# Kernel optimization log

Hardware: AMD Instinct MI355X
Metric: run time of the kernel (lower is better)

## Reference

```python
import jax, jax.numpy as jnp
from jax import lax
import numpy as np

P = 9  # patch_size


def unfold9(img):
    # img: (C, H, W) -> (C, P*P, L) with L = (H//P)*(W//P), non-overlapping patches
    C, H, W = img.shape
    x = img.reshape(C, H // P, P, W // P, P)
    x = x.transpose(0, 2, 4, 1, 3).reshape(C, P * P, (H // P) * (W // P))
    return x


def fold9(blocks, H, W):
    # blocks: (C, P*P, L) -> (C, H, W), inverse of unfold9 (no overlaps)
    C = blocks.shape[0]
    x = blocks.reshape(C, P, P, H // P, W // P)
    return x.transpose(0, 3, 1, 4, 2).reshape(C, H, W)


def avgpool3d_k3s2p1(x):
    # AvgPool3d(kernel=3, stride=2, padding=1, count_include_pad=False) on (B,C,D,H,W)
    win = (1, 1, 3, 3, 3)
    strides = (1, 1, 2, 2, 2)
    pad = [(0, 0), (0, 0), (1, 1), (1, 1), (1, 1)]
    s = lax.reduce_window(x, 0.0, lax.add, win, strides, pad)
    cnt = lax.reduce_window(jnp.ones_like(x[:1, :1]), 0.0, lax.add, win, strides, pad)
    return s / cnt


def setup_inputs() -> dict:
    key = jax.random.key(0)
    k = jax.random.split(key, 7)
    in1, in2, out = 32, 64, 64
    x = jax.random.normal(k[0], (1, in1, 36, 72, 72), jnp.float32)
    y = jax.random.normal(k[1], (1, in2, 18, 36, 36), jnp.float32)
    z = jax.random.normal(k[2], (1, out, 36, 72, 72), jnp.float32)
    w_img = jax.random.normal(k[3], (out, in1), jnp.float32) * 0.05
    b_img = jax.random.normal(k[4], (out,), jnp.float32) * 0.01
    w_fea = jax.random.normal(k[5], (out, in2), jnp.float32) * 0.05
    b_fea = jax.random.normal(k[6], (out,), jnp.float32) * 0.01
    return {"x": x, "y": y, "z": z, "w_img": w_img, "b_img": b_img,
            "w_fea": w_fea, "b_fea": b_fea}


def reference(x, y, z, w_img, b_img, w_fea, b_fea):
    # 1x1x1 conv projections (pointwise channel mix)
    xq = jnp.einsum('bcdhw,oc->bodhw', x, w_img) + b_img[None, :, None, None, None]
    yk = jnp.einsum('bcdhw,oc->bodhw', y, w_fea) + b_fea[None, :, None, None, None]
    C = xq.shape[1]
    D1, HW1 = xq.shape[2], xq.shape[3] * xq.shape[4]
    D2, HW2 = yk.shape[2], yk.shape[3] * yk.shape[4]
    Ux = unfold9(xq.reshape(C, D1, HW1))          # (C, 81, L1)
    Uy = unfold9(yk.reshape(C, D2, HW2))          # (C, 81, L2)
    att = jnp.einsum('ckl,ckm->clm', Ux, Uy)      # (C, L1, L2) per-channel patch attn

    # --- Cross_head ---
    Dd, Hd, Wd = z.shape[2], z.shape[3], z.shape[4]
    dec = z.reshape(C, Dd, Hd * Wd)               # decoder_reshape
    xd = avgpool3d_k3s2p1(z)                      # (1, C, Dd', Hd', Wd')
    Dp, HWp = xd.shape[2], xd.shape[3] * xd.shape[4]
    Uxd = unfold9(xd.reshape(C, Dp, HWp))         # (C, 81, L2)
    # count_nonzero along L2 (non-differentiable, matches torch)
    nz = jnp.sum(att != 0, axis=-1).astype(att.dtype) + 1e-5  # (C, L1)
    corr_blocks = jnp.einsum('clm,ckm->ckl', att / nz[:, :, None], Uxd)  # (C, 81, L1)
    corr = fold9(corr_blocks, Dd, Hd * Wd)        # (C, Dd, Hd*Wd)
    act = jnp.where(corr > 0, corr, 0.2 * corr)   # LeakyReLU(0.2)
    out = act * dec + dec
    return out.reshape(z.shape)
```

## Files before the change

kernel.cpp:

```cpp
#include <hip/hip_runtime.h>
#include <hip/hip_bf16.h>

typedef __hip_bfloat16 bf16;
typedef float in_t;
typedef float out_t;
typedef __attribute__((ext_vector_type(8))) short short8;
typedef __attribute__((ext_vector_type(4))) float f32x4;

#define CH    64
#define CIN1  32
#define CIN2  64
#define S1    186624
#define W1    5184
#define S2    23328
#define W2    1296
#define LDSTR 1297
#define BSTR  104
#define OSTR  136
#define YSTR  68
#define HWSTR 76
#define INV_NZ (1.0f/(288.0f + 1e-5f))

#define NB_PL 2304
#define NB_PX 1458
#define NB_PY 365
#define NBT   (NB_PL + NB_PX + NB_PY)
#define NBR   (NBT - NB_PL)

static __device__ __forceinline__ unsigned short f2bu(float f) {
    bf16 h = __float2bfloat16(f);
    unsigned short u;
    __builtin_memcpy(&u, &h, 2);
    return u;
}
static __device__ __forceinline__ float bu2f(unsigned short u) {
    unsigned int v = ((unsigned int)u) << 16;
    float f;
    __builtin_memcpy(&f, &v, 4);
    return f;
}

__global__ __launch_bounds__(256) void k_stage1(
    const in_t* __restrict__ x, const in_t* __restrict__ wi, const in_t* __restrict__ bi,
    bf16* __restrict__ xq,
    const in_t* __restrict__ y, const in_t* __restrict__ wf, const in_t* __restrict__ bf,
    unsigned short* __restrict__ yk,
    const in_t* __restrict__ z, unsigned short* __restrict__ xd)
{
    __shared__ __align__(16) char smem[17408];
    int t = threadIdx.x;
    long long i = blockIdx.x;

    long long pb = (i*NB_PL)/NBT;
    bool is_pool = ((i+1)*NB_PL)/NBT > pb;
    long long r  = i - pb;
    long long yb = (r*NB_PY)/NBR;
    bool is_py   = !is_pool && (((r+1)*NB_PY)/NBR > yb);

    if (is_pool) {
        int bid = (int)pb;
        float* dsum = reinterpret_cast<float*>(smem);
        int c  = bid / 36;
        int rr = bid - c*36;
        int od = rr >> 1, half = rr & 1;
        int hbase = half ? 35 : 0;
        int nrows = half ? 37 : 36;
        int oh0   = half ? 18 : 0;
        int dlo = od ? 2*od - 1 : 0;
        int nd  = od ? 3 : 2;
        const float* zb = z + ((size_t)c*36 + dlo)*W1;
        for (int ii = t; ii < nrows*18; ii += 256) {
            int rw = ii / 18, q = ii - (ii/18)*18;
            int off = (hbase + rw)*18 + q;
            const float4* p0 = reinterpret_cast<const float4*>(zb);
            float4 a = p0[off], b = p0[1296 + off];
            float4 s;
            if (nd == 3) {
                float4 e = p0[2592 + off];
                s = (float4){ a.x+b.x+e.x, a.y+b.y+e.y, a.z+b.z+e.z, a.w+b.w+e.w };
            } else {
                s = (float4){ a.x+b.x, a.y+b.y, a.z+b.z, a.w+b.w };
            }
            *reinterpret_cast<float4*>(&dsum[rw*HWSTR + q*4]) = s;
        }
        __syncthreads();
        float icd = (nd == 3) ? (1.f/3.f) : 0.5f;
        unsigned short* xdp = xd + (size_t)c*S2 + (size_t)od*W2 + oh0*36;
        for (int idx = t; idx < 648; idx += 256) {
            int ohl = idx / 36, ow = idx - (idx/36)*36;
            int oh = oh0 + ohl;
            int h0 = oh ? 2*oh-1 : 0, h1 = 2*oh+1;
            int w0 = ow ? 2*ow-1 : 0, w1 = 2*ow+1;
            float s = 0.f;
            for (int h = h0; h <= h1; ++h) {
                int lr = h - hbase;
                for (int w = w0; w <= w1; ++w)
                    s += dsum[lr*HWSTR + w];
            }
            float ich = (h1 - h0) == 1 ? 0.5f : (1.f/3.f);
            float icw = (w1 - w0) == 1 ? 0.5f : (1.f/3.f);
            xdp[idx] = f2bu(s * icd * ich * icw);
        }
    } else if (!is_py) {
        int gs0 = (int)(r - yb)*128;
        int l = t & 63, wv = t >> 6;
        int lcol = l & 15, loct = l >> 4;

        ushort4 rr4[2][4];
        #pragma unroll
        for (int mt = 0; mt < 2; ++mt) {
            int scol = gs0 + (wv*2 + mt)*16 + lcol;
            union { short8 v; unsigned short u[8]; } af;
            #pragma unroll
            for (int j = 0; j < 8; ++j)
                af.u[j] = f2bu(x[(size_t)(loct*8 + j)*S1 + scol]);
            #pragma unroll
            for (int og = 0; og < 4; ++og) {
                int o = og*16 + lcol;
                union { short8 v; unsigned short u[8]; } wfr;
                float4 a  = *reinterpret_cast<const float4*>(&wi[o*CIN1 + loct*8]);
                float4 bq = *reinterpret_cast<const float4*>(&wi[o*CIN1 + loct*8 + 4]);
                wfr.u[0]=f2bu(a.x);  wfr.u[1]=f2bu(a.y);
                wfr.u[2]=f2bu(a.z);  wfr.u[3]=f2bu(a.w);
                wfr.u[4]=f2bu(bq.x); wfr.u[5]=f2bu(bq.y);
                wfr.u[6]=f2bu(bq.z); wfr.u[7]=f2bu(bq.w);
                float bo = bi[o];
                f32x4 d = { bo, bo, bo, bo };
                d = __builtin_amdgcn_mfma_f32_16x16x32_bf16(af.v, wfr.v, d, 0, 0, 0);
                rr4[mt][og] = (ushort4){ f2bu(d[0]), f2bu(d[1]), f2bu(d[2]), f2bu(d[3]) };
            }
        }
        unsigned short* ot = reinterpret_cast<unsigned short*>(smem);
        #pragma unroll
        for (int mt = 0; mt < 2; ++mt)
            #pragma unroll
            for (int og = 0; og < 4; ++og)
                *reinterpret_cast<ushort4*>(
                    &ot[(og*16 + lcol)*OSTR + wv*32 + mt*16 + loct*4]) = rr4[mt][og];
        __syncthreads();
        #pragma unroll
        for (int j = 0; j < 4; ++j) {
            int row = wv*16 + j*4 + (l >> 4);
            int c8  = l & 15;
            uint4 v = *reinterpret_cast<const uint4*>(&ot[row*OSTR + c8*8]);
            *reinterpret_cast<uint4*>(
                (unsigned short*)xq + (size_t)row*S1 + gs0 + c8*8) = v;
        }
    } else {
        int pyb   = (int)yb;
        int sblk0 = pyb*64;
        int wv = t >> 6, l = t & 63;
        int lcol = l & 15, loct = l >> 4;
        int tile = pyb*4 + wv;
        unsigned short* ot = reinterpret_cast<unsigned short*>(smem);
        if (tile < 1458) {
            int s0 = tile*16;
            union { short8 v; unsigned short u[8]; } af[2];
            #pragma unroll
            for (int kk = 0; kk < 2; ++kk)
                #pragma unroll
                for (int j = 0; j < 8; ++j)
                    af[kk].u[j] = f2bu(y[(size_t)(kk*32 + loct*8 + j)*S2 + s0 + lcol]);
            #pragma unroll
            for (int og = 0; og < 4; ++og) {
                int o = og*16 + lcol;
                union { short8 v; unsigned short u[8]; } wfr[2];
                #pragma unroll
                for (int kk = 0; kk < 2; ++kk) {
                    float4 a  = *reinterpret_cast<const float4*>(&wf[o*CIN2 + kk*32 + loct*8]);
                    float4 bq = *reinterpret_cast<const float4*>(&wf[o*CIN2 + kk*32 + loct*8 + 4]);
                    wfr[kk].u[0]=f2bu(a.x);  wfr[kk].u[1]=f2bu(a.y);
                    wfr[kk].u[2]=f2bu(a.z);  wfr[kk].u[3]=f2bu(a.w);
                    wfr[kk].u[4]=f2bu(bq.x); wfr[kk].u[5]=f2bu(bq.y);
                    wfr[kk].u[6]=f2bu(bq.z); wfr[kk].u[7]=f2bu(bq.w);
                }
                float bo = bf[o];
                f32x4 d = { bo, bo, bo, bo };
                d = __builtin_amdgcn_mfma_f32_16x16x32_bf16(af[0].v, wfr[0].v, d, 0, 0, 0);
                d = __builtin_amdgcn_mfma_f32_16x16x32_bf16(af[1].v, wfr[1].v, d, 0, 0, 0);
                ushort4 r4 = { f2bu(d[0]), f2bu(d[1]), f2bu(d[2]), f2bu(d[3]) };
                *reinterpret_cast<ushort4*>(&ot[(og*16 + lcol)*YSTR + wv*16 + loct*4]) = r4;
            }
        }
        __syncthreads();
        #pragma unroll
        for (int j = 0; j < 4; ++j) {
            int row = wv*16 + j*4 + (l >> 4);
            int c4  = l & 15;
            int s   = sblk0 + c4*4;
            if (s < S2) {
                ushort4 v = *reinterpret_cast<const ushort4*>(&ot[row*YSTR + c4*4]);
                *reinterpret_cast<ushort4*>(&yk[(size_t)row*S2 + s]) = v;
            }
        }
    }
}

__global__ __launch_bounds__(256) void k_M(
    const unsigned short* __restrict__ xd, const unsigned short* __restrict__ yk,
    unsigned short* __restrict__ Mg)
{
    __shared__ float xl[3*LDSTR];
    __shared__ float yl[3*LDSTR];
    int b = blockIdx.x;
    int c = b / 9, r = b - c*9;
    int g = r / 3, h = r - g*3;
    int t = threadIdx.x;
    int t1 = t / 27, t2 = t - (t/27)*27;
    int offx[3];
    #pragma unroll
    for (int a = 0; a < 3; ++a) {
        int kl = t1*3 + a;
        offx[a] = (kl/9)*LDSTR + (kl - (kl/9)*9);
    }
    int offy = (t2/9)*LDSTR + (t2 - (t2/9)*9);
    float acc[3] = {};
    for (int ph2 = 0; ph2 < 2; ++ph2) {
        __syncthreads();
        for (int idx = t; idx < 3*W2; idx += 256) {
            int rr = idx / W2, col = idx - rr*W2;
            xl[rr*LDSTR + col] = bu2f(xd[c*S2 + (ph2*9 + g*3 + rr)*W2 + col]);
            yl[rr*LDSTR + col] = bu2f(yk[c*S2 + (ph2*9 + h*3 + rr)*W2 + col]);
        }
        __syncthreads();
        if (t < 243) {
            for (int m = 0; m < 144; ++m) {
                int cb = m*9;
                float yv = yl[cb + offy];
                #pragma unroll
                for (int a = 0; a < 3; ++a)
                    acc[a] += xl[cb + offx[a]] * yv;
            }
        }
    }
    if (t < 243) {
        #pragma unroll
        for (int a = 0; a < 3; ++a) {
            int k1 = g*27 + t1*3 + a;
            Mg[c*9216 + k1*96 + (h*27 + t2)] = f2bu(acc[a]);
        }
    }
    if (r == 0) {
        for (int idx = t; idx < 2655; idx += 256) {
            int row, col;
            if (idx < 1440) { int q = idx/96; row = 81 + q; col = idx - q*96; }
            else { int j = idx - 1440; int q = j/15; row = q; col = 81 + (j - q*15); }
            Mg[c*9216 + row*96 + col] = 0;
        }
    }
}

__global__ __launch_bounds__(256, 4) void k_corr(
    const unsigned short* __restrict__ Mg, const bf16* __restrict__ xq,
    const in_t* __restrict__ z, out_t* __restrict__ out)
{
    __shared__ __align__(16) unsigned short Pl[192*BSTR];
    int bid = blockIdx.x;
    int c   = bid / 12;
    int rem = bid - c*12;
    int ph  = rem / 3;
    int ck  = rem - ph*3;
    int colbase = ck*1728;
    int t = threadIdx.x;

    for (int idx = t; idx < 192*15; idx += 256) {
        int r = idx/15;
        Pl[r*BSTR + 81 + (idx - r*15)] = 0;
    }
    const unsigned short* xqu =
        (const unsigned short*)(xq + (size_t)c*S1 + (size_t)(ph*9)*W1 + colbase);
    for (int idx = t; idx < 3888; idx += 256) {
        int i2 = idx / 432, v4 = idx - i2*432;
        ushort4 vv = *reinterpret_cast<const ushort4*>(xqu + (size_t)i2*W1 + v4*4);
        int col = v4*4;
        unsigned short uu[4] = {vv.x, vv.y, vv.z, vv.w};
        #pragma unroll
        for (int j = 0; j < 4; ++j) {
            int cc = col + j;
            int p = cc/9, j2 = cc - p*9;
            Pl[p*BSTR + i2*9 + j2] = uu[j];
        }
    }
    __syncthreads();

    int wv = t >> 6, l = t & 63;
    int lrow = l & 15, lhi = l >> 4;

    short8 bfr[3][3];
    #pragma unroll
    for (int ntl = 0; ntl < 3; ++ntl) {
        int n = (wv*3 + ntl)*16 + lrow;
        #pragma unroll
        for (int kk = 0; kk < 3; ++kk)
            bfr[ntl][kk] = *reinterpret_cast<const short8*>(&Pl[n*BSTR + kk*32 + lhi*8]);
    }

    f32x4 acc[6][3];
    #pragma unroll
    for (int mt = 0; mt < 6; ++mt)
        #pragma unroll
        for (int ntl = 0; ntl < 3; ++ntl)
            acc[mt][ntl] = (f32x4){0.f,0.f,0.f,0.f};

    const unsigned short* Mc = Mg + c*9216;
    #pragma unroll
    for (int mt = 0; mt < 6; ++mt) {
        short8 afr[3];
        #pragma unroll
        for (int kk = 0; kk < 3; ++kk)
            afr[kk] = *reinterpret_cast<const short8*>(Mc + (mt*16 + lrow)*96 + kk*32 + lhi*8);
        #pragma unroll
        for (int ntl = 0; ntl < 3; ++ntl) {
            f32x4 d = acc[mt][ntl];
            #pragma unroll
            for (int kk = 0; kk < 3; ++kk)
                d = __builtin_amdgcn_mfma_f32_16x16x32_bf16(afr[kk], bfr[ntl][kk], d, 0, 0, 0);
            acc[mt][ntl] = d;
        }
    }
    __syncthreads();

    float* stage = reinterpret_cast<float*>(Pl);
    #pragma unroll
    for (int pass = 0; pass < 2; ++pass) {
        if ((wv >> 1) == pass) {
            #pragma unroll
            for (int mt = 0; mt < 6; ++mt)
                #pragma unroll
                for (int ntl = 0; ntl < 3; ++ntl) {
                    int n = (wv*3 + ntl)*16 + lrow - pass*96;
                    #pragma unroll
                    for (int r = 0; r < 4; ++r) {
                        int m = mt*16 + lhi*4 + r;
                        if (m <= 80) {
                            int i = m/9, j = m - 9*i;
                            stage[i*864 + n*9 + j] = acc[mt][ntl][r];
                        }
                    }
                }
        }
        __syncthreads();
        for (int idx = t; idx < 1944; idx += 256) {
            int i = idx/216, c4 = idx - i*216;
            float4 sv = *reinterpret_cast<const float4*>(&stage[i*864 + c4*4]);
            int ga = c*S1 + (ph*9 + i)*W1 + colbase + pass*864 + c4*4;
            float4 dv = *reinterpret_cast<const float4*>(&z[ga]);
            float4 ov;
            float cr;
            cr = sv.x*INV_NZ; ov.x = dv.x + (cr > 0.f ? cr : 0.2f*cr)*dv.x;
            cr = sv.y*INV_NZ; ov.y = dv.y + (cr > 0.f ? cr : 0.2f*cr)*dv.y;
            cr = sv.z*INV_NZ; ov.z = dv.z + (cr > 0.f ? cr : 0.2f*cr)*dv.z;
            cr = sv.w*INV_NZ; ov.w = dv.w + (cr > 0.f ? cr : 0.2f*cr)*dv.w;
            *reinterpret_cast<float4*>(&out[ga]) = ov;
        }
        __syncthreads();
    }
}

extern "C" void kernel_launch(void* const* d_in, const int* in_sizes, int n_in,
                              void* d_out, int out_size, void* d_ws, size_t ws_size,
                              hipStream_t stream)
{
    (void)in_sizes; (void)n_in; (void)out_size; (void)ws_size;
    const in_t* x     = (const in_t*)d_in[0];
    const in_t* y     = (const in_t*)d_in[1];
    const in_t* z     = (const in_t*)d_in[2];
    const in_t* w_img = (const in_t*)d_in[3];
    const in_t* b_img = (const in_t*)d_in[4];
    const in_t* w_fea = (const in_t*)d_in[5];
    const in_t* b_fea = (const in_t*)d_in[6];
    out_t* out = (out_t*)d_out;

    char* ws = (char*)d_ws;
    bf16*           xq = (bf16*)          (ws + 0);
    unsigned short* yk = (unsigned short*)(ws + 23887872);
    unsigned short* xd = (unsigned short*)(ws + 26873856);
    unsigned short* Mg = (unsigned short*)(ws + 29859840);

    hipLaunchKernelGGL(k_stage1, dim3(NBT), dim3(256), 0, stream,
                       x, w_img, b_img, xq, y, w_fea, b_fea, yk, z, xd);
    hipLaunchKernelGGL(k_M,      dim3(576), dim3(256), 0, stream, xd, yk, Mg);
    hipLaunchKernelGGL(k_corr,   dim3(768), dim3(256), 0, stream, Mg, xq, z, out);
}
```

Baseline: 80.24 us.

## Compute per-channel patch Gram matrix M with bf16 MFMA in one block per channel

Rewrites k_M so each channel's 96x96 (padded 81x81) matrix M = Uxd·Uyᵀ is computed by a single block using 16x16x32 bf16 MFMA instructions. xd and yk tiles are staged into LDS in patch-major layout instead of fp32 scalar FMAs. The grid drops from 576 to 64 blocks, so less of the GPU is occupied but the redundant reloads across 9 sub-blocks go away. Zero padding rows and columns are produced by the MFMA tile itself rather than by separate stores.

```diff
diff --git a/kernel.cpp b/kernel.cpp
--- a/kernel.cpp
+++ b/kernel.cpp
@@ -14,8 +14,8 @@
 #define W1    5184
 #define S2    23328
 #define W2    1296
-#define LDSTR 1297
 #define BSTR  104
+#define ASTR  104
 #define OSTR  136
 #define YSTR  68
 #define HWSTR 76
@@ -32,12 +32,6 @@
     unsigned short u;
     __builtin_memcpy(&u, &h, 2);
     return u;
-}
-static __device__ __forceinline__ float bu2f(unsigned short u) {
-    unsigned int v = ((unsigned int)u) << 16;
-    float f;
-    __builtin_memcpy(&f, &v, 4);
-    return f;
 }
 
 __global__ __launch_bounds__(256) void k_stage1(
@@ -200,54 +194,80 @@
     const unsigned short* __restrict__ xd, const unsigned short* __restrict__ yk,
     unsigned short* __restrict__ Mg)
 {
-    __shared__ float xl[3*LDSTR];
-    __shared__ float yl[3*LDSTR];
-    int b = blockIdx.x;
-    int c = b / 9, r = b - c*9;
-    int g = r / 3, h = r - g*3;
+    __shared__ __align__(16) unsigned short Al[96*ASTR];
+    __shared__ __align__(16) unsigned short Bl[96*ASTR];
+    int c = blockIdx.x;
     int t = threadIdx.x;
-    int t1 = t / 27, t2 = t - (t/27)*27;
-    int offx[3];
-    #pragma unroll
-    for (int a = 0; a < 3; ++a) {
-        int kl = t1*3 + a;
-        offx[a] = (kl/9)*LDSTR + (kl - (kl/9)*9);
-    }
-    int offy = (t2/9)*LDSTR + (t2 - (t2/9)*9);
-    float acc[3] = {};
-    for (int ph2 = 0; ph2 < 2; ++ph2) {
-        __syncthreads();
-        for (int idx = t; idx < 3*W2; idx += 256) {
-            int rr = idx / W2, col = idx - rr*W2;
-            xl[rr*LDSTR + col] = bu2f(xd[c*S2 + (ph2*9 + g*3 + rr)*W2 + col]);
-            yl[rr*LDSTR + col] = bu2f(yk[c*S2 + (ph2*9 + h*3 + rr)*W2 + col]);
-        }
-        __syncthreads();
-        if (t < 243) {
-            for (int m = 0; m < 144; ++m) {
-                int cb = m*9;
-                float yv = yl[cb + offy];
+    int l = t & 63, wv = t >> 6;
+    int lcol = l & 15, lhi = l >> 4;
+    int wr = wv >> 1, wc = wv & 1;
+
+    for (int idx = t; idx < 15*ASTR; idx += 256) {
+        Al[81*ASTR + idx] = 0;
+        Bl[81*ASTR + idx] = 0;
+    }
+
+    f32x4 acc[3][3];
+    #pragma unroll
+    for (int a = 0; a < 3; ++a)
+        #pragma unroll
+        for (int b = 0; b < 3; ++b)
+            acc[a][b] = (f32x4){0.f,0.f,0.f,0.f};
+
+    const unsigned short* xc = xd + (size_t)c*S2;
+    const unsigned short* yc = yk + (size_t)c*S2;
+
+    for (int q = 0; q < 3; ++q) {
+        __syncthreads();
+        for (int idx = t; idx < 1944; idx += 256) {
+            int r18 = idx / 108, u4 = idx - r18*108;
+            int srcoff = r18*W2 + q*432 + u4*4;
+            ushort4 va = *reinterpret_cast<const ushort4*>(xc + srcoff);
+            ushort4 vb = *reinterpret_cast<const ushort4*>(yc + srcoff);
+            int ph2 = r18 / 9, i2 = r18 - ph2*9;
+            unsigned short ua[4] = {va.x, va.y, va.z, va.w};
+            unsigned short ub[4] = {vb.x, vb.y, vb.z, vb.w};
+            #pragma unroll
+            for (int j = 0; j < 4; ++j) {
+                int cc  = u4*4 + j;
+                int pw2 = cc / 9, j2 = cc - pw2*9;
+                int row = i2*9 + j2;
+                int mp  = pw2*2 + ph2;
+                Al[row*ASTR + mp] = ua[j];
+                Bl[row*ASTR + mp] = ub[j];
+            }
+        }
+        __syncthreads();
+        #pragma unroll
+        for (int kk = 0; kk < 3; ++kk) {
+            short8 afr[3], bfr[3];
+            #pragma unroll
+            for (int a = 0; a < 3; ++a)
+                afr[a] = *reinterpret_cast<const short8*>(
+                    &Al[(wr*48 + a*16 + lcol)*ASTR + kk*32 + lhi*8]);
+            #pragma unroll
+            for (int b = 0; b < 3; ++b)
+                bfr[b] = *reinterpret_cast<const short8*>(
+                    &Bl[(wc*48 + b*16 + lcol)*ASTR + kk*32 + lhi*8]);
+            #pragma unroll
+            for (int a = 0; a < 3; ++a)
                 #pragma unroll
-                for (int a = 0; a < 3; ++a)
-                    acc[a] += xl[cb + offx[a]] * yv;
-            }
-        }
-    }
-    if (t < 243) {
-        #pragma unroll
-        for (int a = 0; a < 3; ++a) {
-            int k1 = g*27 + t1*3 + a;
-            Mg[c*9216 + k1*96 + (h*27 + t2)] = f2bu(acc[a]);
-        }
-    }
-    if (r == 0) {
-        for (int idx = t; idx < 2655; idx += 256) {
-            int row, col;
-            if (idx < 1440) { int q = idx/96; row = 81 + q; col = idx - q*96; }
-            else { int j = idx - 1440; int q = j/15; row = q; col = 81 + (j - q*15); }
-            Mg[c*9216 + row*96 + col] = 0;
-        }
-    }
+                for (int b = 0; b < 3; ++b)
+                    acc[a][b] = __builtin_amdgcn_mfma_f32_16x16x32_bf16(
+                        afr[a], bfr[b], acc[a][b], 0, 0, 0);
+        }
+    }
+    unsigned short* Mc = Mg + (size_t)c*9216;
+    #pragma unroll
+    for (int a = 0; a < 3; ++a)
+        #pragma unroll
+        for (int b = 0; b < 3; ++b)
+            #pragma unroll
+            for (int rr = 0; rr < 4; ++rr) {
+                int k1 = wr*48 + a*16 + lhi*4 + rr;
+                int k2 = wc*48 + b*16 + lcol;
+                Mc[k1*96 + k2] = f2bu(acc[a][b][rr]);
+            }
 }
 
 __global__ __launch_bounds__(256, 4) void k_corr(
@@ -379,6 +399,6 @@
 
     hipLaunchKernelGGL(k_stage1, dim3(NBT), dim3(256), 0, stream,
                        x, w_img, b_img, xq, y, w_fea, b_fea, yk, z, xd);
-    hipLaunchKernelGGL(k_M,      dim3(576), dim3(256), 0, stream, xd, yk, Mg);
+    hipLaunchKernelGGL(k_M,      dim3(64),  dim3(256), 0, stream, xd, yk, Mg);
     hipLaunchKernelGGL(k_corr,   dim3(768), dim3(256), 0, stream, Mg, xq, z, out);
 }
```

New measurement: 66.26 us (median of 2 runs). 1.21x faster.
